# Kernel tuning notes

Hardware: AMD Instinct MI355X
Metric: run time of the kernel (lower is better)

Reference implementation:

```python
import jax, jax.numpy as jnp
import numpy as np

EPS = 1e-3
D_MIN, D_MAX = 3.0, 80.0   # z_near, z_far
NUM_FREQS = 6              # -> code dim 3*(1+2*6)=39; 64+39=103 total

N_, NV_, C_, H_, W_ = 4, 4, 64, 96, 320
N_PTS = 50000


def posenc(x):
    # pixelnerf-style positional encoding with include_input, d_in=3
    freqs = jnp.asarray(np.pi * 2.0 ** np.arange(NUM_FREQS), dtype=x.dtype)
    xb = x[..., None, :] * freqs[:, None]                      # [..., F, 3]
    enc = jnp.stack([jnp.sin(xb), jnp.cos(xb)], axis=-2)       # [..., F, 2, 3]
    enc = enc.reshape(x.shape[:-1] + (NUM_FREQS * 2 * 3,))
    return jnp.concatenate([x, enc], axis=-1)                  # [..., 39]


def grid_sample_bilinear_border(fm, xy):
    # fm: [N, C, H, W], xy: [N, P, 2] in [-1, 1]; align_corners=False, border pad
    N, C, H, W = fm.shape
    x = jnp.clip(((xy[..., 0] + 1.0) * W - 1.0) * 0.5, 0.0, W - 1.0)
    y = jnp.clip(((xy[..., 1] + 1.0) * H - 1.0) * 0.5, 0.0, H - 1.0)
    x0 = jnp.floor(x); y0 = jnp.floor(y)
    wx = (x - x0)[:, None, :]; wy = (y - y0)[:, None, :]       # [N, 1, P]
    x0i = x0.astype(jnp.int32); y0i = y0.astype(jnp.int32)
    x1i = jnp.minimum(x0i + 1, W - 1); y1i = jnp.minimum(y0i + 1, H - 1)
    gather = jax.vmap(lambda f, yi, xi: f[:, yi, xi])          # [C, P] per batch
    v00 = gather(fm, y0i, x0i)
    v01 = gather(fm, y0i, x1i)
    v10 = gather(fm, y1i, x0i)
    v11 = gather(fm, y1i, x1i)
    return (v00 * (1 - wx) * (1 - wy) + v01 * wx * (1 - wy)
            + v10 * (1 - wx) * wy + v11 * wx * wy)             # [N, C, P]


def setup_inputs() -> dict:
    key = jax.random.key(0)
    k = jax.random.split(key, 5)
    return {
        "xyz": jax.random.normal(k[0], (N_, N_PTS, 3), jnp.float32),
        "feature_map": jax.random.normal(k[1], (N_, NV_, C_, H_, W_), jnp.float32),
        "poses_w2c": jax.random.normal(k[2], (N_, NV_, 4, 4), jnp.float32),
        "Ks": jax.random.normal(k[3], (N_, NV_, 3, 3), jnp.float32),
        "empty_feature": jax.random.normal(k[4], (C_,), jnp.float32),
    }


def reference(xyz, feature_map, poses_w2c, Ks, empty_feature):
    n, n_pts, _ = xyz.shape
    n, nv, c, h, w = feature_map.shape
    # homogeneous points, project to each camera
    xyzh = jnp.concatenate([xyz, jnp.ones_like(xyz[..., :1])], axis=-1)  # [n,P,4]
    xyz_cam = jnp.einsum('nvij,npj->nvpi', poses_w2c[:, :, :3, :], xyzh)  # [n,nv,P,3]
    proj = jnp.einsum('nvij,nvpj->nvpi', Ks, xyz_cam)                    # [n,nv,P,3]
    z = proj[..., 2:3]
    xy = proj[..., :2] / jnp.maximum(z, EPS)
    invalid = ((z <= EPS) | (xy[..., :1] < -1) | (xy[..., :1] > 1)
               | (xy[..., 1:2] < -1) | (xy[..., 1:2] > 1))               # [n,nv,P,1]
    # code_mode='z', inv_z=True
    z_code = (1.0 / jnp.maximum(z, EPS) - 1.0 / D_MAX) / (1.0 / D_MIN - 1.0 / D_MAX)
    z_code = 2.0 * z_code - 1.0
    code = posenc(jnp.concatenate([xy, z_code], axis=-1))                # [n,nv,P,39]
    code = code.transpose(0, 2, 1, 3)                                    # [n,P,nv,39]
    sampled = grid_sample_bilinear_border(
        feature_map.reshape(n * nv, c, h, w), xy.reshape(n * nv, n_pts, 2))
    sampled = sampled.reshape(n, nv, c, n_pts).transpose(0, 3, 1, 2)     # [n,P,nv,c]
    inv_t = invalid.transpose(0, 2, 1, 3)                                # [n,P,nv,1]
    sampled = jnp.where(inv_t, empty_feature, sampled)                   # learn_empty
    feats = jnp.concatenate([sampled, code], axis=-1)                    # [n,P,nv,103]
    return feats, invalid[..., 0].transpose(0, 2, 1)                     # [n,P,nv]
```

## Files before the change

kernel.cpp:

```cpp
#include <hip/hip_runtime.h>
#include <hip/hip_bf16.h>


#define EPSF 0.001f
constexpr int N_ = 4, NV_ = 4, C_ = 64, H_ = 96, W_ = 320, NPTS = 50000;
constexpr int HW = H_ * W_;
constexpr int FEAT = 103;
constexpr int TOTAL_PTS = N_ * NPTS;
constexpr long long FEATS_TOTAL = (long long)TOTAL_PTS * NV_ * FEAT;
constexpr size_t TFM_ELEMS = (size_t)N_ * NV_ * HW * C_;
constexpr int BLOCKS = 2048;

__global__ __launch_bounds__(256) void transpose_fm(const float* __restrict__ fm,
                                                    unsigned char* __restrict__ tfm) {
    __shared__ float tile[64][65];
    const int s    = blockIdx.y;
    const int pos0 = blockIdx.x * 64;
    const int t    = threadIdx.x;
    const int lane = t & 63, q = t >> 6;

    const float* src = fm + (size_t)s * C_ * HW;
#pragma unroll
    for (int i = 0; i < 16; ++i) {
        const int c = q * 16 + i;
        tile[c][lane] = __builtin_nontemporal_load(&src[(size_t)c * HW + pos0 + lane]);
    }
    __syncthreads();
    const int g  = t & 15;
    const int pr = t >> 4;
    unsigned int* dstU = (unsigned int*)(tfm + ((size_t)s * HW + pos0) * C_);
#pragma unroll
    for (int i = 0; i < 4; ++i) {
        const int pos = i * 16 + pr;
        const float f0 = tile[4 * g + 0][pos];
        const float f1 = tile[4 * g + 1][pos];
        const float f2 = tile[4 * g + 2][pos];
        const float f3 = tile[4 * g + 3][pos];
        unsigned w = (unsigned)__builtin_amdgcn_cvt_pk_fp8_f32(f0, f1, 0, false);
        w = (unsigned)__builtin_amdgcn_cvt_pk_fp8_f32(f2, f3, (int)w, true);
        dstU[pos * (C_ / 4) + g] = w;
    }
}

template <bool DIRECT>
__global__ __launch_bounds__(256, 8) void mvbts_main(const float* __restrict__ xyz,
                                                     const float* __restrict__ fmapF,
                                                     const unsigned char* __restrict__ fmapB,
                                                     const float* __restrict__ poses,
                                                     const float* __restrict__ Ks,
                                                     const float* __restrict__ ef,
                                                     float* __restrict__ out) {
    __shared__ float  PKall[N_][NV_][21];
    __shared__ int4   offsS[256];
    __shared__ float4 wS[256];
    __shared__ float4 auxS[256];

    const int t    = threadIdx.x;
    const int lane = t & 63;
    const int v    = t >> 6;

    for (int e = t; e < N_ * NV_ * 21; e += 256) {
        const int nn = e / (NV_ * 21), r = e - nn * (NV_ * 21);
        const int vv = r / 21, k = r - vv * 21;
        float val;
        if (k < 12) val = poses[((size_t)(nn * NV_ + vv) * 4 + (k >> 2)) * 4 + (k & 3)];
        else        val = Ks[(size_t)(nn * NV_ + vv) * 9 + (k - 12)];
        PKall[nn][vv][k] = val;
    }

    const int jj = lane - 3;
    const int f6 = (lane >= 3) ? (jj / 6) : 0;
    const int r6 = (lane >= 3) ? (jj - f6 * 6) : 0;
    const int tt = (r6 >= 3) ? 1 : 0;
    const int ci = (lane < 3) ? lane : (r6 - tt * 3);
    const float pf  = (lane < 3) ? 0.f : 3.14159265358979f * (float)(1 << f6);
    const float qtr = (lane >= 3 && tt) ? 1.57079632679490f : 0.f;
    const float efv = ef[lane];

    const int s0 = (int)(((long long)blockIdx.x * TOTAL_PTS) >> 11);
    const int s1 = (int)(((long long)(blockIdx.x + 1) * TOTAL_PTS) >> 11);

    for (int c0 = s0; c0 < s1; c0 += 64) {
        const int cl = min(64, s1 - c0);
        __syncthreads();

        {
            const int P  = c0 + lane;
            const int Pl = min(P, TOTAL_PTS - 1);
            const int n  = Pl / NPTS;
            const float X = xyz[(size_t)Pl * 3 + 0];
            const float Y = xyz[(size_t)Pl * 3 + 1];
            const float Z = xyz[(size_t)Pl * 3 + 2];

            const float* pk = PKall[n][v];
            float cam[3], prj[3];
#pragma unroll
            for (int i = 0; i < 3; ++i)
                cam[i] = __fadd_rn(
                           __fadd_rn(__fadd_rn(__fmul_rn(pk[i * 4 + 0], X),
                                               __fmul_rn(pk[i * 4 + 1], Y)),
                                     __fmul_rn(pk[i * 4 + 2], Z)),
                           pk[i * 4 + 3]);
#pragma unroll
            for (int i = 0; i < 3; ++i)
                prj[i] = __fadd_rn(__fadd_rn(__fmul_rn(pk[12 + i * 3 + 0], cam[0]),
                                             __fmul_rn(pk[12 + i * 3 + 1], cam[1])),
                                   __fmul_rn(pk[12 + i * 3 + 2], cam[2]));

            const float pz = prj[2];
            const float zc = fmaxf(pz, EPSF);
            const float x  = __fdiv_rn(prj[0], zc);
            const float y  = __fdiv_rn(prj[1], zc);
            const bool invalid = (pz <= EPSF) || (x < -1.f) || (x > 1.f) || (y < -1.f) || (y > 1.f);

            const float zinv = __fdiv_rn(1.f, zc);
            float z_code = __fdiv_rn(zinv - 0.0125f, (1.f / 3.f - 0.0125f));
            z_code = 2.f * z_code - 1.f;

            float gx = fminf(fmaxf(((x + 1.f) * (float)W_ - 1.f) * 0.5f, 0.f), (float)(W_ - 1));
            float gy = fminf(fmaxf(((y + 1.f) * (float)H_ - 1.f) * 0.5f, 0.f), (float)(H_ - 1));
            const float fx0 = floorf(gx), fy0 = floorf(gy);
            const int x0 = (int)fx0, y0 = (int)fy0;
            const int x1 = min(x0 + 1, W_ - 1), y1 = min(y0 + 1, H_ - 1);
            const float wx = gx - fx0, wy = gy - fy0;
            const float vmask = invalid ? 0.f : 1.f;
            const float owx = 1.f - wx, owy = 1.f - wy;
            const int scl = DIRECT ? 1 : C_;
            const int sbase = (n * NV_ + v) * (HW * C_);
            int4 o;
            o.x = sbase + (y0 * W_ + x0) * scl;
            o.y = sbase + (y0 * W_ + x1) * scl;
            o.z = sbase + (y1 * W_ + x0) * scl;
            o.w = sbase + (y1 * W_ + x1) * scl;
            offsS[t] = o;
            wS[t] = make_float4(vmask * owx * owy, vmask * wx * owy,
                                vmask * owx * wy,  vmask * wx * wy);
            auxS[t] = make_float4(x, y, z_code, invalid ? 1.f : 0.f);

            if (P < s1)
                out[FEATS_TOTAL + (size_t)P * NV_ + v] = invalid ? 1.f : 0.f;
        }
        __syncthreads();

        const float* blF = DIRECT ? fmapF + (size_t)lane * HW : nullptr;
        unsigned off = ((unsigned)c0 * NV_ + v) * FEAT;
#pragma unroll 2
        for (int i = 0; i < cl; ++i, off += NV_ * FEAT) {
            const int item = (v << 6) + i;
            const int4   o  = offsS[item];
            const float4 w4 = wS[item];
            const float4 a4 = auxS[item];
            float v00, v01, v10, v11;
            if (DIRECT) {
                v00 = blF[o.x]; v01 = blF[o.y]; v10 = blF[o.z]; v11 = blF[o.w];
            } else {
                v00 = __builtin_amdgcn_cvt_f32_fp8((int)fmapB[(unsigned)o.x + lane], 0);
                v01 = __builtin_amdgcn_cvt_f32_fp8((int)fmapB[(unsigned)o.y + lane], 0);
                v10 = __builtin_amdgcn_cvt_f32_fp8((int)fmapB[(unsigned)o.z + lane], 0);
                v11 = __builtin_amdgcn_cvt_f32_fp8((int)fmapB[(unsigned)o.w + lane], 0);
            }
            const float samp = v00 * w4.x + v01 * w4.y + v10 * w4.z + v11 * w4.w
                             + a4.w * efv;
            out[off + lane] = samp;

            if (lane < 39) {
                const float b = (ci == 0) ? a4.x : ((ci == 1) ? a4.y : a4.z);
                const float tv = __sinf(b * pf + qtr);
                out[off + 64 + lane] = (lane < 3) ? b : tv;
            }
        }
    }
}

extern "C" void kernel_launch(void* const* d_in, const int* in_sizes, int n_in,
                              void* d_out, int out_size, void* d_ws, size_t ws_size,
                              hipStream_t stream) {
    const float* xyz   = (const float*)d_in[0];
    const float* fm    = (const float*)d_in[1];
    const float* poses = (const float*)d_in[2];
    const float* Ks    = (const float*)d_in[3];
    const float* ef    = (const float*)d_in[4];
    float* out = (float*)d_out;

    const size_t need = TFM_ELEMS;
    if (ws_size >= need) {
        unsigned char* tfm = (unsigned char*)d_ws;
        transpose_fm<<<dim3(HW / 64, N_ * NV_), 256, 0, stream>>>(fm, tfm);
        mvbts_main<false><<<dim3(BLOCKS), 256, 0, stream>>>(xyz, nullptr, tfm, poses, Ks, ef, out);
    } else {
        mvbts_main<true><<<dim3(BLOCKS), 256, 0, stream>>>(xyz, fm, nullptr, poses, Ks, ef, out);
    }
}
```

Baseline: 114.9 us.

## Gather four fp8 channels per lane and process four points per wavefront iteration

```diff
diff --git a/kernel.cpp b/kernel.cpp
--- a/kernel.cpp
+++ b/kernel.cpp
@@ -10,6 +10,8 @@
 constexpr long long FEATS_TOTAL = (long long)TOTAL_PTS * NV_ * FEAT;
 constexpr size_t TFM_ELEMS = (size_t)N_ * NV_ * HW * C_;
 constexpr int BLOCKS = 2048;
+
+typedef float v2f __attribute__((__vector_size__(8)));
 
 __global__ __launch_bounds__(256) void transpose_fm(const float* __restrict__ fm,
                                                     unsigned char* __restrict__ tfm) {
@@ -68,17 +70,12 @@
         PKall[nn][vv][k] = val;
     }
 
-    const int jj = lane - 3;
-    const int f6 = (lane >= 3) ? (jj / 6) : 0;
-    const int r6 = (lane >= 3) ? (jj - f6 * 6) : 0;
-    const int tt = (r6 >= 3) ? 1 : 0;
-    const int ci = (lane < 3) ? lane : (r6 - tt * 3);
-    const float pf  = (lane < 3) ? 0.f : 3.14159265358979f * (float)(1 << f6);
-    const float qtr = (lane >= 3 && tt) ? 1.57079632679490f : 0.f;
-    const float efv = ef[lane];
-
     const int s0 = (int)(((long long)blockIdx.x * TOTAL_PTS) >> 11);
     const int s1 = (int)(((long long)(blockIdx.x + 1) * TOTAL_PTS) >> 11);
+
+    const int pt4 = lane >> 4;
+    const int q   = lane & 15;
+    const unsigned laneRowOff = (unsigned)pt4 * NV_ * FEAT;
 
     for (int c0 = s0; c0 < s1; c0 += 64) {
         const int cl = min(64, s1 - c0);
@@ -133,8 +130,10 @@
             o.z = sbase + (y1 * W_ + x0) * scl;
             o.w = sbase + (y1 * W_ + x1) * scl;
             offsS[t] = o;
-            wS[t] = make_float4(vmask * owx * owy, vmask * wx * owy,
-                                vmask * owx * wy,  vmask * wx * wy);
+            float w00 = vmask * owx * owy;
+            if (invalid) w00 = -1.f;
+            wS[t] = make_float4(w00, vmask * wx * owy,
+                                vmask * owx * wy, vmask * wx * wy);
             auxS[t] = make_float4(x, y, z_code, invalid ? 1.f : 0.f);
 
             if (P < s1)
@@ -142,31 +141,94 @@
         }
         __syncthreads();
 
-        const float* blF = DIRECT ? fmapF + (size_t)lane * HW : nullptr;
-        unsigned off = ((unsigned)c0 * NV_ + v) * FEAT;
+        if constexpr (!DIRECT) {
+            const float4 efq = *(const float4*)&ef[4 * q];
+            const unsigned ch = 4u * q;
 #pragma unroll 2
-        for (int i = 0; i < cl; ++i, off += NV_ * FEAT) {
-            const int item = (v << 6) + i;
-            const int4   o  = offsS[item];
-            const float4 w4 = wS[item];
-            const float4 a4 = auxS[item];
-            float v00, v01, v10, v11;
-            if (DIRECT) {
-                v00 = blF[o.x]; v01 = blF[o.y]; v10 = blF[o.z]; v11 = blF[o.w];
-            } else {
-                v00 = __builtin_amdgcn_cvt_f32_fp8((int)fmapB[(unsigned)o.x + lane], 0);
-                v01 = __builtin_amdgcn_cvt_f32_fp8((int)fmapB[(unsigned)o.y + lane], 0);
-                v10 = __builtin_amdgcn_cvt_f32_fp8((int)fmapB[(unsigned)o.z + lane], 0);
-                v11 = __builtin_amdgcn_cvt_f32_fp8((int)fmapB[(unsigned)o.w + lane], 0);
-            }
-            const float samp = v00 * w4.x + v01 * w4.y + v10 * w4.z + v11 * w4.w
-                             + a4.w * efv;
-            out[off + lane] = samp;
-
-            if (lane < 39) {
-                const float b = (ci == 0) ? a4.x : ((ci == 1) ? a4.y : a4.z);
-                const float tv = __sinf(b * pf + qtr);
-                out[off + 64 + lane] = (lane < 3) ? b : tv;
+            for (int i0 = 0; i0 < cl; i0 += 4) {
+                const int pt  = i0 + pt4;
+                const bool ok = pt < cl;
+                const int item = (v << 6) + min(pt, cl - 1);
+                const int4   o  = offsS[item];
+                const float4 w4 = wS[item];
+                const unsigned g00 = *(const unsigned*)(fmapB + (unsigned)o.x + ch);
+                const unsigned g01 = *(const unsigned*)(fmapB + (unsigned)o.y + ch);
+                const unsigned g10 = *(const unsigned*)(fmapB + (unsigned)o.z + ch);
+                const unsigned g11 = *(const unsigned*)(fmapB + (unsigned)o.w + ch);
+                const float flag = (w4.x < 0.f) ? 1.f : 0.f;
+                const float w00  = fmaxf(w4.x, 0.f);
+                const v2f l00 = __builtin_amdgcn_cvt_pk_f32_fp8((int)g00, false);
+                const v2f h00 = __builtin_amdgcn_cvt_pk_f32_fp8((int)g00, true);
+                const v2f l01 = __builtin_amdgcn_cvt_pk_f32_fp8((int)g01, false);
+                const v2f h01 = __builtin_amdgcn_cvt_pk_f32_fp8((int)g01, true);
+                const v2f l10 = __builtin_amdgcn_cvt_pk_f32_fp8((int)g10, false);
+                const v2f h10 = __builtin_amdgcn_cvt_pk_f32_fp8((int)g10, true);
+                const v2f l11 = __builtin_amdgcn_cvt_pk_f32_fp8((int)g11, false);
+                const v2f h11 = __builtin_amdgcn_cvt_pk_f32_fp8((int)g11, true);
+                const float s0v = l00[0] * w00 + l01[0] * w4.y + l10[0] * w4.z + l11[0] * w4.w + flag * efq.x;
+                const float s1v = l00[1] * w00 + l01[1] * w4.y + l10[1] * w4.z + l11[1] * w4.w + flag * efq.y;
+                const float s2v = h00[0] * w00 + h01[0] * w4.y + h10[0] * w4.z + h11[0] * w4.w + flag * efq.z;
+                const float s3v = h00[1] * w00 + h01[1] * w4.y + h10[1] * w4.z + h11[1] * w4.w + flag * efq.w;
+                const unsigned ro = ((unsigned)(c0 + i0) * NV_ + v) * FEAT + laneRowOff + ch;
+                if (ok) {
+                    out[ro + 0] = s0v;
+                    out[ro + 1] = s1v;
+                    out[ro + 2] = s2v;
+                    out[ro + 3] = s3v;
+                }
+            }
+            float pfc[4], qtc[4]; int cic[4]; bool rawc[4], okc[4];
+#pragma unroll
+            for (int jjj = 0; jjj < 4; ++jjj) {
+                const int j = 4 * q + jjj;
+                okc[jjj] = (j < 39);
+                if (j < 3) { cic[jjj] = j; rawc[jjj] = true; pfc[jjj] = 0.f; qtc[jjj] = 0.f; }
+                else {
+                    const int f = (j - 3) / 6, r = (j - 3) % 6;
+                    const bool cosf_ = (r >= 3);
+                    cic[jjj] = cosf_ ? (r - 3) : r; rawc[jjj] = false;
+                    pfc[jjj] = 3.14159265358979f * (float)(1 << f);
+                    qtc[jjj] = cosf_ ? 1.57079632679490f : 0.f;
+                }
+            }
+            for (int i0 = 0; i0 < cl; i0 += 4) {
+                const int pt  = i0 + pt4;
+                const bool ok = pt < cl;
+                const float4 a4 = auxS[(v << 6) + min(pt, cl - 1)];
+                const unsigned ro = ((unsigned)(c0 + i0) * NV_ + v) * FEAT + laneRowOff + 64 + 4 * q;
+#pragma unroll
+                for (int jjj = 0; jjj < 4; ++jjj) {
+                    const float b = (cic[jjj] == 0) ? a4.x : ((cic[jjj] == 1) ? a4.y : a4.z);
+                    const float val = rawc[jjj] ? b : __sinf(b * pfc[jjj] + qtc[jjj]);
+                    if (ok && okc[jjj]) out[ro + jjj] = val;
+                }
+            }
+        } else {
+            const float* blF = fmapF + (size_t)lane * HW;
+            const int jj = lane - 3;
+            const int f6 = (lane >= 3) ? (jj / 6) : 0;
+            const int r6 = (lane >= 3) ? (jj - f6 * 6) : 0;
+            const int tt = (r6 >= 3) ? 1 : 0;
+            const int ci = (lane < 3) ? lane : (r6 - tt * 3);
+            const float pf  = (lane < 3) ? 0.f : 3.14159265358979f * (float)(1 << f6);
+            const float qtr = (lane >= 3 && tt) ? 1.57079632679490f : 0.f;
+            const float efv = ef[lane];
+            unsigned off = ((unsigned)c0 * NV_ + v) * FEAT;
+            for (int i = 0; i < cl; ++i, off += NV_ * FEAT) {
+                const int item = (v << 6) + i;
+                const int4   o  = offsS[item];
+                const float4 w4 = wS[item];
+                const float4 a4 = auxS[item];
+                const float flag = (w4.x < 0.f) ? 1.f : 0.f;
+                const float w00  = fmaxf(w4.x, 0.f);
+                const float v00 = blF[o.x], v01 = blF[o.y], v10 = blF[o.z], v11 = blF[o.w];
+                const float samp = v00 * w00 + v01 * w4.y + v10 * w4.z + v11 * w4.w + flag * efv;
+                out[off + lane] = samp;
+                if (lane < 39) {
+                    const float b = (ci == 0) ? a4.x : ((ci == 1) ? a4.y : a4.z);
+                    const float tv = __sinf(b * pf + qtr);
+                    out[off + 64 + lane] = (lane < 3) ? b : tv;
+                }
             }
         }
     }
```

New measurement: 175.1 us. 52.4% more time.
